# Kernel optimization log

Measured on AMD Instinct MI355X. Metric: run time of the kernel, lower is better.

The kernel has to match this reference:

```python
import jax, jax.numpy as jnp
import numpy as np
from jax import lax

ANGRES = 5


def _conv(x, w, stride=(1, 1), pad=((1, 1), (1, 1)), dil=(1, 1)):
    return lax.conv_general_dilated(x, w, stride, pad, rhs_dilation=dil,
                                    dimension_numbers=('NCHW', 'OIHW', 'NCHW'))


def _lrelu(x):
    return jnp.where(x >= 0, x, 0.1 * x)


def _block_s(x, w):
    # SAI input: split into 5x5 grid of (sh,sw) views, conv each view, emit MacPI-interleaved layout
    B, C, H, W = x.shape
    sh, sw = H // 5, W // 5
    p = x.reshape(B, C, 5, sh, 5, sw).transpose(0, 2, 4, 1, 3, 5).reshape(B * 25, C, sh, sw)
    y = _conv(p, w).reshape(B, 5, 5, C, sh, sw)
    # (B,bi,bj,C,sh,sw) -> (B,C,sh,bi,sw,bj) -> (B,C,H,W)   [torch permute(0,3,4,1,5,2)]
    return y.transpose(0, 3, 4, 1, 5, 2).reshape(B, C, H, W)


def _block_a(x, w):
    # MacPI input: conv each 5x5 macropixel independently (zero pad at block edges)
    B, C, H, W = x.shape
    nh, nw = H // 5, W // 5
    p = x.reshape(B, C, nh, 5, nw, 5).transpose(0, 2, 4, 1, 3, 5).reshape(B * nh * nw, C, 5, 5)
    y = _conv(p, w)
    return y.reshape(B, nh, nw, C, 5, 5).transpose(0, 3, 1, 4, 2, 5).reshape(B, C, H, W)


def _epi(x, w1, w2, a):
    # EPI conv: [1,3a] kernel, stride [1,a], pad [0,a]; then 1x1 to a*C; then 1D pixel shuffle on W
    y = _lrelu(_conv(x, w1, stride=(1, a), pad=((0, 0), (a, a))))
    y = _lrelu(_conv(y, w2, pad=((0, 0), (0, 0))))
    B, aC, H, Wa = y.shape
    C = aC // a
    return y.reshape(B, a, C, H, Wa).transpose(0, 2, 3, 4, 1).reshape(B, C, H, Wa * a)


def _att_fuse(buf, alpha, gamma, beta, eps=1e-5):
    # covariance-based GLU attention over the N=4 branches
    B, NC, H, W = buf.shape
    N = 4
    C = NC // N
    x5 = buf.reshape(B, N, C, H, W)
    xr = x5.reshape(B, N, C * H * W)
    M = xr.shape[-1]
    xc = xr - jnp.mean(xr, axis=-1, keepdims=True)
    cov = jnp.einsum('bnm,bkm->bnk', xc, xc) * (alpha / (M - 1))  # [B,N,N]
    norm = cov / jnp.sqrt(jnp.mean(cov * cov, axis=(1, 2), keepdims=True) + eps)
    g = gamma * norm + beta
    att = g * jax.nn.sigmoid(g)  # GLU of duplicated halves
    out = jnp.einsum('bnk,bkm->bnm', att, xr).reshape(B, N, C, H, W) + x5
    return out.reshape(B, NC, H, W)


def _mac2sai(x, a):
    B, C, HU, WV = x.shape
    h, w = HU // a, WV // a
    return x.reshape(B, C, a, h, a, w).transpose(0, 1, 3, 5, 2, 4).reshape(B, C, h * a, w * a)


def _tsfefb(x, x1, ws, wa, we1, we2, al, ga, be, wf1, wf2, a):
    feaSpa = _lrelu(_block_s(x1, ws))
    feaAng = _lrelu(_block_a(x, wa))
    feaH = _epi(x, we1, we2, a)
    feaV = jnp.transpose(_epi(jnp.transpose(x, (0, 1, 3, 2)), we1, we2, a), (0, 1, 3, 2))
    buf = jnp.concatenate([feaSpa, feaAng, feaH, feaV], axis=1)
    out = _att_fuse(buf, al, ga, be)
    y = _lrelu(_conv(out, wf1, pad=((0, 0), (0, 0))))
    y = _conv(y, wf2, pad=((a, a), (a, a)), dil=(a, a))
    return y + x


def setup_inputs() -> dict:
    key = jax.random.key(0)
    ks = jax.random.split(key, 12)
    B, C, a, n = 4, 64, ANGRES, 4
    H = W = a * 32  # 160

    def w(k, shape):
        fan_in = float(np.prod(shape[2:]))
        return jax.random.normal(k, shape, jnp.float32) / np.float32(np.sqrt(fan_in))

    return {
        'x': jax.random.normal(ks[0], (B, C, H, W), jnp.float32),
        'x1': jax.random.normal(ks[1], (B, C, H, W), jnp.float32),
        'w_spa': w(ks[2], (n, C, C, 3, 3)),
        'w_ang': w(ks[3], (n, C, C, 3, 3)),
        'w_epi1': w(ks[4], (n, C, C, 1, 3 * a)),
        'w_epi2': w(ks[5], (n, a * C, C, 1, 1)),
        'alpha': jnp.ones((n,), jnp.float32),
        'gamma': 0.1 * jax.random.normal(ks[6], (n,), jnp.float32),
        'beta': 0.1 * jax.random.normal(ks[7], (n,), jnp.float32),
        'w_fuse1': w(ks[8], (n, C, 4 * C, 1, 1)),
        'w_fuse2': w(ks[9], (n, C, C, 3, 3)),
    }


def reference(x, x1, w_spa, w_ang, w_epi1, w_epi2, alpha, gamma, beta, w_fuse1, w_fuse2):
    a = ANGRES
    buf, buf1 = x, x1
    for i in range(w_spa.shape[0]):
        buf = _tsfefb(buf, buf1, w_spa[i], w_ang[i], w_epi1[i], w_epi2[i],
                      alpha[i], gamma[i], beta[i], w_fuse1[i], w_fuse2[i], a)
        buf1 = _mac2sai(buf, a)
    return buf
```

## Files before the change

### kernel.cpp

```cpp
#include <hip/hip_runtime.h>

__device__ __forceinline__ float lrelu(float v){ return v >= 0.f ? v : 0.1f*v; }


__global__ __launch_bounds__(256) void k_spa(const float* __restrict__ buf1, const float* __restrict__ w,
                                             float* __restrict__ out){
  const int P = blockIdx.x;
  const int within = P >> 3, cog = within & 7, tsel = within >> 3;
  const int tg = (P & 7)*25 + tsel;
  const int b = tg / 50, r2 = tg % 50;
  const int view = r2 >> 1, half = r2 & 1;
  const int bi = view / 5, bj = view % 5;
  const int th0 = half*16;
  const int tid = threadIdx.x;
  __shared__ float plane[2][18*38];
  for (int idx=tid; idx<2*18*38; idx+=256) ((float*)plane)[idx]=0.f;
  float acc[2][8];
  #pragma unroll
  for (int k=0;k<2;k++)
    #pragma unroll
    for (int c=0;c<8;c++) acc[k][c]=0.f;
  const float* src = buf1 + (size_t)b*1638400 + bi*32*160 + bj*32;
  const float* wb = w + (size_t)(cog*8)*576;
  const int sr = tid >> 3, sq = (tid & 7)*4;
  const int vr = th0 - 1 + sr;
  const bool rowok = (tid < 144) && ((unsigned)vr < 32u);
  __syncthreads();
  if (rowok)
    *(float4*)&plane[0][sr*38 + 4 + sq] = *(const float4*)(src + vr*160 + sq);
  __syncthreads();
  const int lr = tid >> 5, c = tid & 31;
  for (int ci=0; ci<64; ci++){
    float4 nx;
    const bool ld = rowok && (ci < 63);
    if (ld) nx = *(const float4*)(src + (size_t)(ci+1)*25600 + vr*160 + sq);
    const float* P2 = plane[ci & 1];
    float t0[9], t1[9];
    {
      const float* pp = &P2[lr*38 + c + 3];
      t0[0]=pp[0];  t0[1]=pp[1];  t0[2]=pp[2];
      t0[3]=pp[38]; t0[4]=pp[39]; t0[5]=pp[40];
      t0[6]=pp[76]; t0[7]=pp[77]; t0[8]=pp[78];
      const float* qq = pp + 8*38;
      t1[0]=qq[0];  t1[1]=qq[1];  t1[2]=qq[2];
      t1[3]=qq[38]; t1[4]=qq[39]; t1[5]=qq[40];
      t1[6]=qq[76]; t1[7]=qq[77]; t1[8]=qq[78];
    }
    #pragma unroll
    for (int co=0;co<8;co++){
      const float* wp = wb + (size_t)co*576 + ci*9;
      float w0=wp[0],w1=wp[1],w2=wp[2],w3=wp[3],w4=wp[4],w5=wp[5],w6=wp[6],w7=wp[7],w8=wp[8];
      acc[0][co] += t0[0]*w0+t0[1]*w1+t0[2]*w2+t0[3]*w3+t0[4]*w4
                  + t0[5]*w5+t0[6]*w6+t0[7]*w7+t0[8]*w8;
      acc[1][co] += t1[0]*w0+t1[1]*w1+t1[2]*w2+t1[3]*w3+t1[4]*w4
                  + t1[5]*w5+t1[6]*w6+t1[7]*w7+t1[8]*w8;
    }
    if (ld) *(float4*)&plane[(ci+1)&1][sr*38 + 4 + sq] = nx;
    __syncthreads();
  }
  #pragma unroll
  for (int k=0;k<2;k++){
    int si = th0 + lr + k*8;
    int h = si*5 + bi, wq = c*5 + bj;
    #pragma unroll
    for (int co=0;co<8;co++){
      int ch = b*64 + cog*8 + co;
      out[(size_t)ch*25600 + h*160 + wq] = lrelu(acc[k][co]);
    }
  }
}

__global__ __launch_bounds__(320) void k_ang(const float* __restrict__ bufA, const float* __restrict__ w,
                                             float* __restrict__ out){
  const int P = blockIdx.x;
  const int within = P >> 3, cog = within & 15, tsel = within >> 4;
  const int tg = (P & 7)*8 + tsel;
  const int b = tg >> 4, mip = tg & 15;
  const int tid = threadIdx.x;
  __shared__ float lds[2][2296];
  for (int i=tid; i<2*2296; i+=320) ((float*)lds)[i] = 0.f;

  const int u = tid >> 6, mi_l = (tid >> 5) & 1, mp = tid & 31;
  int ro[3];
  #pragma unroll
  for (int du=0; du<3; du++)
    ro[du] = mi_l*1148 + (u+du)*164 + mp*5;
  const bool st1 = tid < 80;
  const int rr0 = tid/40,       q0 = tid%40;
  const int rr1 = (tid+320)/40, q1 = (tid+320)%40;
  const int dst0 = (rr0/5)*1148 + (1 + rr0%5)*164 + q0*4;
  const int dst1 = (rr1/5)*1148 + (1 + rr1%5)*164 + q1*4;
  const float* src = bufA + (size_t)b*1638400 + (size_t)(mip*10)*160;
  const float* wb = w + (size_t)(cog*4)*576;

  float acc[4][5];
  #pragma unroll
  for (int co=0;co<4;co++)
    #pragma unroll
    for (int v=0;v<5;v++) acc[co][v]=0.f;

  __syncthreads();
  {
    *(float4*)&lds[0][dst0] = *(const float4*)(src + rr0*160 + q0*4);
    if (st1)
      *(float4*)&lds[0][dst1] = *(const float4*)(src + rr1*160 + q1*4);
  }
  __syncthreads();
  for (int ci=0; ci<64; ci++){
    float4 n0, n1;
    if (ci < 63){
      n0 = *(const float4*)(src + (size_t)(ci+1)*25600 + rr0*160 + q0*4);
      if (st1) n1 = *(const float4*)(src + (size_t)(ci+1)*25600 + rr1*160 + q1*4);
    }
    const float* Pb = lds[ci & 1];
    float c[3][5];
    #pragma unroll
    for (int du=0;du<3;du++){
      const float* rp = &Pb[ro[du]];
      c[du][0]=rp[0]; c[du][1]=rp[1]; c[du][2]=rp[2]; c[du][3]=rp[3]; c[du][4]=rp[4];
    }
    #pragma unroll
    for (int co=0;co<4;co++){
      const float* wp = wb + (size_t)co*576 + ci*9;
      float w0=wp[0],w1=wp[1],w2=wp[2],w3=wp[3],w4=wp[4],w5=wp[5],w6=wp[6],w7=wp[7],w8=wp[8];
      acc[co][0] += c[0][0]*w1 + c[0][1]*w2
                  + c[1][0]*w4 + c[1][1]*w5
                  + c[2][0]*w7 + c[2][1]*w8;
      acc[co][1] += c[0][0]*w0 + c[0][1]*w1 + c[0][2]*w2
                  + c[1][0]*w3 + c[1][1]*w4 + c[1][2]*w5
                  + c[2][0]*w6 + c[2][1]*w7 + c[2][2]*w8;
      acc[co][2] += c[0][1]*w0 + c[0][2]*w1 + c[0][3]*w2
                  + c[1][1]*w3 + c[1][2]*w4 + c[1][3]*w5
                  + c[2][1]*w6 + c[2][2]*w7 + c[2][3]*w8;
      acc[co][3] += c[0][2]*w0 + c[0][3]*w1 + c[0][4]*w2
                  + c[1][2]*w3 + c[1][3]*w4 + c[1][4]*w5
                  + c[2][2]*w6 + c[2][3]*w7 + c[2][4]*w8;
      acc[co][4] += c[0][3]*w0 + c[0][4]*w1
                  + c[1][3]*w3 + c[1][4]*w4
                  + c[2][3]*w6 + c[2][4]*w7;
    }
    if (ci < 63){
      float* Q = lds[(ci+1)&1];
      *(float4*)&Q[dst0] = n0;
      if (st1) *(float4*)&Q[dst1] = n1;
    }
    __syncthreads();
  }
  const int h = (mip*2 + mi_l)*5 + u;
  const int wc0 = mp*5;
  #pragma unroll
  for (int co=0;co<4;co++){
    int ch = b*64 + cog*4 + co;
    float* op = out + (size_t)ch*25600 + (size_t)h*160 + wc0;
    op[0]=lrelu(acc[co][0]); op[1]=lrelu(acc[co][1]); op[2]=lrelu(acc[co][2]);
    op[3]=lrelu(acc[co][3]); op[4]=lrelu(acc[co][4]);
  }
}

__global__ __launch_bounds__(320) void k_epi(const float* __restrict__ bufA, const float* __restrict__ we1,
                                             const float* __restrict__ we2, float* __restrict__ out){
  const int bb = blockIdx.x >> 1, half = blockIdx.x & 1;
  const int b = bb / 160, hw = bb % 160;
  const int tid = threadIdx.x;
  __shared__ float rowp[64*96];
  __shared__ float y1s[64*16];
  const int lofs = half ? 0 : 8;
  const int xofs = half ? 72 : 0;
  for (int ft=tid; ft<1408; ft+=320){
    int ci = ft/22, q = ft - ci*22;
    *(float4*)&rowp[ci*96 + lofs + q*4] =
      *(const float4*)(bufA + (size_t)b*1638400 + (size_t)ci*25600 + (size_t)hw*160 + xofs + q*4);
  }
  for (int idx=tid; idx<512; idx+=320){
    int ci = idx>>3, j = idx&7;
    rowp[ci*96 + (half ? 88+j : j)] = 0.f;
  }
  __syncthreads();
  if (tid < 256){
    const int co = tid >> 2, wvl0 = (tid & 3)*4;
    const int a0 = 2 + wvl0*5;
    float acc[4];
    #pragma unroll
    for (int j=0;j<4;j++) acc[j]=0.f;
    const float* wp0 = we1 + (size_t)co*960;
    for (int ci=0; ci<64; ci++){
      float fl[32];
      const float* rp = &rowp[ci*96 + a0];
      #pragma unroll
      for (int m=0;m<16;m++) *(float2*)&fl[2*m] = *(const float2*)&rp[2*m];
      const float* wp = wp0 + ci*15;
      #pragma unroll
      for (int t=0;t<15;t++){
        float wt = wp[t];
        #pragma unroll
        for (int j=0;j<4;j++) acc[j] += fl[1 + j*5 + t]*wt;
      }
    }
    #pragma unroll
    for (int j=0;j<4;j++) y1s[co*16 + wvl0 + j] = lrelu(acc[j]);
  }
  __syncthreads();
  {
    const int oc = tid, kk = oc >> 6, c = oc & 63;
    float a2[16];
    #pragma unroll
    for (int wv=0;wv<16;wv++) a2[wv]=0.f;
    const float* wp = we2 + (size_t)oc*64;
    for (int ci=0; ci<64; ci++){
      float wt = wp[ci];
      const float* yp = &y1s[ci*16];
      #pragma unroll
      for (int wv=0; wv<16; wv++) a2[wv] += yp[wv]*wt;
    }
    float* y2s = rowp;
    #pragma unroll
    for (int wv=0; wv<16; wv++) y2s[c*84 + wv*5 + kk] = lrelu(a2[wv]);
  }
  __syncthreads();
  {
    const float* y2s = rowp;
    for (int k=0;k<4;k++){
      int f = (tid + k*320)*4;
      int c = f/80, rr = f - c*80;
      *(float4*)(out + (size_t)(b*64+c)*25600 + (size_t)hw*160 + half*80 + rr)
        = *(const float4*)&y2s[c*84+rr];
    }
  }
}

__global__ __launch_bounds__(256) void k_permV(const float* __restrict__ tmp, float* __restrict__ dst){
  const int bc = blockIdx.x;
  const int ti = blockIdx.y / 5, tj = blockIdx.y % 5;
  const int hw0 = ti*32, r0 = tj*32;
  const int lx = threadIdx.x & 31, ly = threadIdx.x >> 5;
  __shared__ float tile[32][33];
  const float* in = tmp + (size_t)bc*25600;
  float* outp = dst + (size_t)bc*25600;
  for (int yy=ly; yy<32; yy+=8)
    tile[yy][lx] = in[(size_t)(hw0+yy)*160 + r0 + lx];
  __syncthreads();
  for (int yy=ly; yy<32; yy+=8)
    outp[(size_t)(r0+yy)*160 + hw0 + lx] = tile[lx][yy];
}

__global__ __launch_bounds__(256) void k_permM(const float* __restrict__ A, float* __restrict__ dst){
  const int bc = blockIdx.x >> 5, hh = blockIdx.x & 31;
  const int tid = threadIdx.x;
  __shared__ float rows[5*160];
  const float* in = A + (size_t)bc*25600;
  if (tid < 200){
    int ai = tid/40, q = (tid - ai*40)*4;
    *(float4*)&rows[ai*160 + q] = *(const float4*)(in + (size_t)(ai*32+hh)*160 + q);
  }
  __syncthreads();
  float* outp = dst + (size_t)bc*25600 + (size_t)hh*800;
  for (int t=tid; t<800; t+=256){
    int ww = t/25, r2 = t - ww*25, ai = r2/5, aj = r2 - ai*5;
    outp[t] = rows[ai*160 + aj*32 + ww];
  }
}

__global__ __launch_bounds__(256) void k_red(const float* __restrict__ b0, const float* __restrict__ b1,
                                             const float* __restrict__ b2, const float* __restrict__ b3,
                                             float* __restrict__ part){
  const int b = blockIdx.y, blk = blockIdx.x;
  const int tid = threadIdx.x;
  const size_t off = (size_t)b*1638400 + (size_t)blk*25600;
  float s0=0,s1=0,s2=0,s3=0;
  float p00=0,p01=0,p02=0,p03=0,p11=0,p12=0,p13=0,p22=0,p23=0,p33=0;
  for (int it=0; it<25; it++){
    size_t m = off + it*1024 + tid*4;
    float4 x0 = *(const float4*)(b0+m);
    float4 x1 = *(const float4*)(b1+m);
    float4 x2 = *(const float4*)(b2+m);
    float4 x3 = *(const float4*)(b3+m);
    s0 += (x0.x+x0.y)+(x0.z+x0.w);
    s1 += (x1.x+x1.y)+(x1.z+x1.w);
    s2 += (x2.x+x2.y)+(x2.z+x2.w);
    s3 += (x3.x+x3.y)+(x3.z+x3.w);
    p00 += x0.x*x0.x+x0.y*x0.y+x0.z*x0.z+x0.w*x0.w;
    p01 += x0.x*x1.x+x0.y*x1.y+x0.z*x1.z+x0.w*x1.w;
    p02 += x0.x*x2.x+x0.y*x2.y+x0.z*x2.z+x0.w*x2.w;
    p03 += x0.x*x3.x+x0.y*x3.y+x0.z*x3.z+x0.w*x3.w;
    p11 += x1.x*x1.x+x1.y*x1.y+x1.z*x1.z+x1.w*x1.w;
    p12 += x1.x*x2.x+x1.y*x2.y+x1.z*x2.z+x1.w*x2.w;
    p13 += x1.x*x3.x+x1.y*x3.y+x1.z*x3.z+x1.w*x3.w;
    p22 += x2.x*x2.x+x2.y*x2.y+x2.z*x2.z+x2.w*x2.w;
    p23 += x2.x*x3.x+x2.y*x3.y+x2.z*x3.z+x2.w*x3.w;
    p33 += x3.x*x3.x+x3.y*x3.y+x3.z*x3.z+x3.w*x3.w;
  }
  float vals[14] = {s0,s1,s2,s3,p00,p01,p02,p03,p11,p12,p13,p22,p23,p33};
  __shared__ float red[4][14];
  int lane = tid & 63, wv = tid >> 6;
  #pragma unroll
  for (int j=0;j<14;j++){
    float v = vals[j];
    #pragma unroll
    for (int o=32;o>0;o>>=1) v += __shfl_down(v,o,64);
    if (lane==0) red[wv][j]=v;
  }
  __syncthreads();
  if (tid<14) part[((size_t)b*64+blk)*16 + tid] = red[0][tid]+red[1][tid]+red[2][tid]+red[3][tid];
}

__global__ __launch_bounds__(256) void k_attW(const float* __restrict__ part,
        const float* __restrict__ alpha, const float* __restrict__ gamma, const float* __restrict__ beta,
        int iblk, const float* __restrict__ wf1, float* __restrict__ Weff){
  const int b = blockIdx.x, tid = threadIdx.x;
  __shared__ float st[14];
  __shared__ float att[16];
  if (tid<14){
    float t=0;
    for (int blk=0;blk<64;blk++) t += part[((size_t)b*64+blk)*16 + tid];
    st[tid]=t;
  }
  __syncthreads();
  if (tid==0){
    const float M = 1638400.f;
    float s[4] = {st[0],st[1],st[2],st[3]};
    float S[4][4];
    S[0][0]=st[4];  S[0][1]=S[1][0]=st[5];  S[0][2]=S[2][0]=st[6];  S[0][3]=S[3][0]=st[7];
    S[1][1]=st[8];  S[1][2]=S[2][1]=st[9];  S[1][3]=S[3][1]=st[10];
    S[2][2]=st[11]; S[2][3]=S[3][2]=st[12]; S[3][3]=st[13];
    float al=alpha[iblk], ga=gamma[iblk], be=beta[iblk];
    float scale = al/(M-1.f);
    float cov[4][4], ss=0.f;
    for (int n=0;n<4;n++) for (int k=0;k<4;k++){
      float c = (S[n][k] - s[n]*s[k]/M)*scale;
      cov[n][k]=c; ss += c*c;
    }
    float rms = sqrtf(ss/16.f + 1e-5f);
    for (int n=0;n<4;n++) for (int k=0;k<4;k++){
      float g = ga*cov[n][k]/rms + be;
      att[n*4+k] = g/(1.f+expf(-g));
    }
  }
  __syncthreads();
  for (int idx=tid; idx<16384; idx+=256){
    int co=idx>>8, kc=idx&255, k=kc>>6, c=kc&63;
    float v = wf1[co*256+kc];
    #pragma unroll
    for (int n=0;n<4;n++) v += att[n*4+k]*wf1[co*256+n*64+c];
    Weff[(size_t)b*16384+idx] = v;
  }
}

__global__ __launch_bounds__(256) void k_fuse1(const float* b0, const float* __restrict__ b1,
                                               const float* __restrict__ b2, const float* __restrict__ b3,
                                               const float* __restrict__ Weff, float* y64){
  const int tile = blockIdx.x, b = blockIdx.y;
  const int px0 = tile*64;
  const int tid = threadIdx.x;
  const int ti = tid >> 4, tj = tid & 15;
  __shared__ float xs[64][68];
  __shared__ float wt[64][68];
  float acc[4][4];
  #pragma unroll
  for (int i=0;i<4;i++)
    #pragma unroll
    for (int j=0;j<4;j++) acc[i][j]=0.f;
  const float* bptr[4] = {b0,b1,b2,b3};
  for (int kb=0; kb<4; kb++){
    const float* xbk = bptr[kb] + (size_t)b*1638400 + px0;
    const float* wb = Weff + (size_t)b*16384 + kb*64;
    __syncthreads();
    for (int idx=tid; idx<4096; idx+=256){
      int kc=idx>>6, px=idx&63;
      xs[kc][px] = xbk[(size_t)kc*25600 + px];
    }
    for (int idx=tid; idx<4096; idx+=256){
      int co=idx>>6, k2=idx&63;
      wt[k2][co] = wb[co*256 + k2];
    }
    __syncthreads();
    for (int k2=0;k2<64;k2++){
      float4 a = *(const float4*)&wt[k2][ti*4];
      float4 v = *(const float4*)&xs[k2][tj*4];
      acc[0][0]+=a.x*v.x; acc[0][1]+=a.x*v.y; acc[0][2]+=a.x*v.z; acc[0][3]+=a.x*v.w;
      acc[1][0]+=a.y*v.x; acc[1][1]+=a.y*v.y; acc[1][2]+=a.y*v.z; acc[1][3]+=a.y*v.w;
      acc[2][0]+=a.z*v.x; acc[2][1]+=a.z*v.y; acc[2][2]+=a.z*v.z; acc[2][3]+=a.z*v.w;
      acc[3][0]+=a.w*v.x; acc[3][1]+=a.w*v.y; acc[3][2]+=a.w*v.z; acc[3][3]+=a.w*v.w;
    }
  }
  #pragma unroll
  for (int i=0;i<4;i++){
    int co = ti*4 + i;
    float4 o = make_float4(lrelu(acc[i][0]), lrelu(acc[i][1]), lrelu(acc[i][2]), lrelu(acc[i][3]));
    *(float4*)(y64 + ((size_t)(b*64+co))*25600 + px0 + tj*4) = o;
  }
}

template<int FINAL>
__global__ __launch_bounds__(256) void k_fuse2(const float* __restrict__ y64, const float* resid,
                                               const float* __restrict__ w, float* outp){
  const int P = blockIdx.x;
  const int within = P >> 3, cog = within & 7, tsel = within >> 3;
  const int tg = (P & 7)*25 + tsel;
  const int b = tg / 50, tile = tg % 50;
  const int th0 = (tile/5)*16, tw0 = (tile%5)*32;
  const int tid = threadIdx.x;
  __shared__ float plane[2][26*48];
  float acc[2][8];
  #pragma unroll
  for (int k=0;k<2;k++)
    #pragma unroll
    for (int c=0;c<8;c++) acc[k][c]=0.f;
  const float* src = y64 + (size_t)b*1638400;
  const float* wb = w + (size_t)(cog*8)*576;
  const int s0r = tid/12,        s0c = tid - (tid/12)*12;
  const int s1i = tid + 256;
  const int s1r = s1i/12,        s1c = s1i - (s1i/12)*12;
  const bool has1 = tid < 56;
  const int g0h = th0 - 5 + s0r, g0w = tw0 - 8 + s0c*4;
  const int g1h = th0 - 5 + s1r, g1w = tw0 - 8 + s1c*4;
  const bool v0 = ((unsigned)g0h < 160u) && ((unsigned)g0w < 160u);
  const bool v1 = has1 && ((unsigned)g1h < 160u) && ((unsigned)g1w < 160u);
  const int go0 = g0h*160 + g0w, go1 = g1h*160 + g1w;
  const int d0 = s0r*48 + s0c*4, d1 = s1r*48 + s1c*4;
  const float4 z4 = make_float4(0.f,0.f,0.f,0.f);
  {
    float4 x0 = v0 ? *(const float4*)(src + go0) : z4;
    *(float4*)&plane[0][d0] = x0;
    if (has1){
      float4 x1 = v1 ? *(const float4*)(src + go1) : z4;
      *(float4*)&plane[0][d1] = x1;
    }
  }
  __syncthreads();
  const int lr = tid >> 5, c = tid & 31;
  const int tap = lr*48 + c + 3;
  for (int ci=0; ci<64; ci++){
    float4 n0, n1;
    if (ci < 63){
      const float* sN = src + (size_t)(ci+1)*25600;
      n0 = v0 ? *(const float4*)(sN + go0) : z4;
      if (has1) n1 = v1 ? *(const float4*)(sN + go1) : z4;
    }
    const float* Pb = plane[ci & 1];
    float t0[9], t1[9];
    {
      const float* pp = &Pb[tap];
      t0[0]=pp[0];      t0[1]=pp[5];      t0[2]=pp[10];
      t0[3]=pp[240];    t0[4]=pp[245];    t0[5]=pp[250];
      t0[6]=pp[480];    t0[7]=pp[485];    t0[8]=pp[490];
      const float* qq = pp + 8*48;
      t1[0]=qq[0];      t1[1]=qq[5];      t1[2]=qq[10];
      t1[3]=qq[240];    t1[4]=qq[245];    t1[5]=qq[250];
      t1[6]=qq[480];    t1[7]=qq[485];    t1[8]=qq[490];
    }
    #pragma unroll
    for (int co=0;co<8;co++){
      const float* wp = wb + (size_t)co*576 + ci*9;
      float w0=wp[0],w1=wp[1],w2=wp[2],w3=wp[3],w4=wp[4],w5=wp[5],w6=wp[6],w7=wp[7],w8=wp[8];
      acc[0][co] += t0[0]*w0+t0[1]*w1+t0[2]*w2+t0[3]*w3+t0[4]*w4
                  + t0[5]*w5+t0[6]*w6+t0[7]*w7+t0[8]*w8;
      acc[1][co] += t1[0]*w0+t1[1]*w1+t1[2]*w2+t1[3]*w3+t1[4]*w4
                  + t1[5]*w5+t1[6]*w6+t1[7]*w7+t1[8]*w8;
    }
    if (ci < 63){
      float* Q = plane[(ci+1)&1];
      *(float4*)&Q[d0] = n0;
      if (has1) *(float4*)&Q[d1] = n1;
    }
    __syncthreads();
  }
  #pragma unroll
  for (int k=0;k<2;k++){
    int h = th0 + lr + k*8, wq = tw0 + c;
    #pragma unroll
    for (int co=0;co<8;co++){
      int cg = cog*8 + co;
      size_t base = ((size_t)(b*64+cg)*160 + h)*160 + wq;
      outp[base] = acc[k][co] + resid[base];
    }
  }
}

extern "C" void kernel_launch(void* const* d_in, const int* in_sizes, int n_in,
                              void* d_out, int out_size, void* d_ws, size_t ws_size,
                              hipStream_t stream){
  const float* x    = (const float*)d_in[0];
  const float* x1   = (const float*)d_in[1];
  const float* wspa = (const float*)d_in[2];
  const float* wang = (const float*)d_in[3];
  const float* we1  = (const float*)d_in[4];
  const float* we2  = (const float*)d_in[5];
  const float* al   = (const float*)d_in[6];
  const float* ga   = (const float*)d_in[7];
  const float* be   = (const float*)d_in[8];
  const float* wf1  = (const float*)d_in[9];
  const float* wf2  = (const float*)d_in[10];

  char* ws = (char*)d_ws;
  const size_t SLOT = 26214400;
  float* A  = (float*)(ws);
  float* Bv = (float*)(ws +   SLOT);
  float* T1 = (float*)(ws + 2*SLOT);
  float* T2 = (float*)(ws + 3*SLOT);
  float* part = (float*)(ws + 4*SLOT);
  float* Weff = (float*)(ws + 4*SLOT + 16384);
  float* D = (float*)d_out;

  for (int i=0;i<4;i++){
    const float* Asrc  = (i==0) ? x  : (const float*)A;
    const float* B1src = (i==0) ? x1 : (const float*)Bv;
    k_permV<<<dim3(256,25),256,0,stream>>>(Asrc, D);
    k_epi<<<1280,320,0,stream>>>(D, we1 + (size_t)i*61440, we2 + (size_t)i*20480, T2);
    k_spa<<<1600,256,0,stream>>>(B1src, wspa + (size_t)i*36864, T1);
    k_permV<<<dim3(256,25),256,0,stream>>>(T2, Bv);
    k_ang<<<1024,320,0,stream>>>(Asrc, wang + (size_t)i*36864, T2);
    k_epi<<<1280,320,0,stream>>>(Asrc, we1 + (size_t)i*61440, we2 + (size_t)i*20480, D);
    k_red<<<dim3(64,4),256,0,stream>>>(T1, T2, D, Bv, part);
    k_attW<<<4,256,0,stream>>>(part, al, ga, be, i, wf1 + (size_t)i*16384, Weff);
    k_fuse1<<<dim3(400,4),256,0,stream>>>(T1, T2, D, Bv, Weff, T1);
    if (i<3){
      k_fuse2<0><<<1600,256,0,stream>>>(T1, Asrc, wf2 + (size_t)i*36864, A);
      k_permM<<<8192,256,0,stream>>>(A, Bv);
    } else {
      k_fuse2<1><<<1600,256,0,stream>>>(T1, Asrc, wf2 + (size_t)i*36864, D);
    }
  }
}
```

Before: 2.780 ms.

## Repack 3x3 conv weights ci-major and give k_spa adjacent output rows

Adds a pre-pass kernel that transposes the spatial, angular and fuse2 3x3 weights into [ci][co][9] order, so each input-channel iteration reads one contiguous span of weights for the block's output channels instead of strided rows. Separately, k_spa now assigns each thread two vertically adjacent output rows and loads a 4x3 shared-memory window instead of two separate 3x3 windows, sharing the overlapping rows. The cost is one extra launch and extra workspace for the repacked weights each call.

```diff
diff --git a/kernel.cpp b/kernel.cpp
--- a/kernel.cpp
+++ b/kernel.cpp
@@ -2,6 +2,17 @@
 
 __device__ __forceinline__ float lrelu(float v){ return v >= 0.f ? v : 0.1f*v; }
 
+
+__global__ __launch_bounds__(256) void k_wrep(const float* __restrict__ wspa, const float* __restrict__ wang,
+                                              const float* __restrict__ wf2, float* __restrict__ outp){
+  int id = blockIdx.x*256 + threadIdx.x;
+  int t = id / 147456, r = id - t*147456;
+  int i = r / 36864,  e = r - i*36864;
+  int ci = e / 576,   r3 = e - ci*576;
+  int co = r3 / 9,    j = r3 - co*9;
+  const float* src = (t==0 ? wspa : (t==1 ? wang : wf2));
+  outp[id] = src[(size_t)i*36864 + co*576 + ci*9 + j];
+}
 
 __global__ __launch_bounds__(256) void k_spa(const float* __restrict__ buf1, const float* __restrict__ w,
                                              float* __restrict__ out){
@@ -21,7 +32,6 @@
     #pragma unroll
     for (int c=0;c<8;c++) acc[k][c]=0.f;
   const float* src = buf1 + (size_t)b*1638400 + bi*32*160 + bj*32;
-  const float* wb = w + (size_t)(cog*8)*576;
   const int sr = tid >> 3, sq = (tid & 7)*4;
   const int vr = th0 - 1 + sr;
   const bool rowok = (tid < 144) && ((unsigned)vr < 32u);
@@ -29,38 +39,36 @@
   if (rowok)
     *(float4*)&plane[0][sr*38 + 4 + sq] = *(const float4*)(src + vr*160 + sq);
   __syncthreads();
-  const int lr = tid >> 5, c = tid & 31;
+  const int lr2 = tid >> 5, c = tid & 31;
   for (int ci=0; ci<64; ci++){
     float4 nx;
     const bool ld = rowok && (ci < 63);
     if (ld) nx = *(const float4*)(src + (size_t)(ci+1)*25600 + vr*160 + sq);
     const float* P2 = plane[ci & 1];
-    float t0[9], t1[9];
+    float g[4][3];
     {
-      const float* pp = &P2[lr*38 + c + 3];
-      t0[0]=pp[0];  t0[1]=pp[1];  t0[2]=pp[2];
-      t0[3]=pp[38]; t0[4]=pp[39]; t0[5]=pp[40];
-      t0[6]=pp[76]; t0[7]=pp[77]; t0[8]=pp[78];
-      const float* qq = pp + 8*38;
-      t1[0]=qq[0];  t1[1]=qq[1];  t1[2]=qq[2];
-      t1[3]=qq[38]; t1[4]=qq[39]; t1[5]=qq[40];
-      t1[6]=qq[76]; t1[7]=qq[77]; t1[8]=qq[78];
-    }
+      const float* pp = &P2[(2*lr2)*38 + c + 3];
+      g[0][0]=pp[0];   g[0][1]=pp[1];   g[0][2]=pp[2];
+      g[1][0]=pp[38];  g[1][1]=pp[39];  g[1][2]=pp[40];
+      g[2][0]=pp[76];  g[2][1]=pp[77];  g[2][2]=pp[78];
+      g[3][0]=pp[114]; g[3][1]=pp[115]; g[3][2]=pp[116];
+    }
+    const float* wrow = w + ci*576 + cog*72;
     #pragma unroll
     for (int co=0;co<8;co++){
-      const float* wp = wb + (size_t)co*576 + ci*9;
+      const float* wp = wrow + co*9;
       float w0=wp[0],w1=wp[1],w2=wp[2],w3=wp[3],w4=wp[4],w5=wp[5],w6=wp[6],w7=wp[7],w8=wp[8];
-      acc[0][co] += t0[0]*w0+t0[1]*w1+t0[2]*w2+t0[3]*w3+t0[4]*w4
-                  + t0[5]*w5+t0[6]*w6+t0[7]*w7+t0[8]*w8;
-      acc[1][co] += t1[0]*w0+t1[1]*w1+t1[2]*w2+t1[3]*w3+t1[4]*w4
-                  + t1[5]*w5+t1[6]*w6+t1[7]*w7+t1[8]*w8;
+      acc[0][co] += g[0][0]*w0+g[0][1]*w1+g[0][2]*w2+g[1][0]*w3+g[1][1]*w4
+                  + g[1][2]*w5+g[2][0]*w6+g[2][1]*w7+g[2][2]*w8;
+      acc[1][co] += g[1][0]*w0+g[1][1]*w1+g[1][2]*w2+g[2][0]*w3+g[2][1]*w4
+                  + g[2][2]*w5+g[3][0]*w6+g[3][1]*w7+g[3][2]*w8;
     }
     if (ld) *(float4*)&plane[(ci+1)&1][sr*38 + 4 + sq] = nx;
     __syncthreads();
   }
   #pragma unroll
   for (int k=0;k<2;k++){
-    int si = th0 + lr + k*8;
+    int si = th0 + 2*lr2 + k;
     int h = si*5 + bi, wq = c*5 + bj;
     #pragma unroll
     for (int co=0;co<8;co++){
@@ -91,7 +99,6 @@
   const int dst0 = (rr0/5)*1148 + (1 + rr0%5)*164 + q0*4;
   const int dst1 = (rr1/5)*1148 + (1 + rr1%5)*164 + q1*4;
   const float* src = bufA + (size_t)b*1638400 + (size_t)(mip*10)*160;
-  const float* wb = w + (size_t)(cog*4)*576;
 
   float acc[4][5];
   #pragma unroll
@@ -119,9 +126,10 @@
       const float* rp = &Pb[ro[du]];
       c[du][0]=rp[0]; c[du][1]=rp[1]; c[du][2]=rp[2]; c[du][3]=rp[3]; c[du][4]=rp[4];
     }
+    const float* wrow = w + ci*576 + cog*36;
     #pragma unroll
     for (int co=0;co<4;co++){
-      const float* wp = wb + (size_t)co*576 + ci*9;
+      const float* wp = wrow + co*9;
       float w0=wp[0],w1=wp[1],w2=wp[2],w3=wp[3],w4=wp[4],w5=wp[5],w6=wp[6],w7=wp[7],w8=wp[8];
       acc[co][0] += c[0][0]*w1 + c[0][1]*w2
                   + c[1][0]*w4 + c[1][1]*w5
@@ -406,7 +414,6 @@
     #pragma unroll
     for (int c=0;c<8;c++) acc[k][c]=0.f;
   const float* src = y64 + (size_t)b*1638400;
-  const float* wb = w + (size_t)(cog*8)*576;
   const int s0r = tid/12,        s0c = tid - (tid/12)*12;
   const int s1i = tid + 256;
   const int s1r = s1i/12,        s1c = s1i - (s1i/12)*12;
@@ -448,9 +455,10 @@
       t1[3]=qq[240];    t1[4]=qq[245];    t1[5]=qq[250];
       t1[6]=qq[480];    t1[7]=qq[485];    t1[8]=qq[490];
     }
+    const float* wrow = w + ci*576 + cog*72;
     #pragma unroll
     for (int co=0;co<8;co++){
-      const float* wp = wb + (size_t)co*576 + ci*9;
+      const float* wp = wrow + co*9;
       float w0=wp[0],w1=wp[1],w2=wp[2],w3=wp[3],w4=wp[4],w5=wp[5],w6=wp[6],w7=wp[7],w8=wp[8];
       acc[0][co] += t0[0]*w0+t0[1]*w1+t0[2]*w2+t0[3]*w3+t0[4]*w4
                   + t0[5]*w5+t0[6]*w6+t0[7]*w7+t0[8]*w8;
@@ -499,25 +507,31 @@
   float* T2 = (float*)(ws + 3*SLOT);
   float* part = (float*)(ws + 4*SLOT);
   float* Weff = (float*)(ws + 4*SLOT + 16384);
+  float* Wrep = (float*)(ws + 4*SLOT + 16384 + 262144);
+  float* WspaR = Wrep;
+  float* WangR = Wrep + 147456;
+  float* Wf2R  = Wrep + 2*147456;
   float* D = (float*)d_out;
+
+  k_wrep<<<1728,256,0,stream>>>(wspa, wang, wf2, Wrep);
 
   for (int i=0;i<4;i++){
     const float* Asrc  = (i==0) ? x  : (const float*)A;
     const float* B1src = (i==0) ? x1 : (const float*)Bv;
     k_permV<<<dim3(256,25),256,0,stream>>>(Asrc, D);
     k_epi<<<1280,320,0,stream>>>(D, we1 + (size_t)i*61440, we2 + (size_t)i*20480, T2);
-    k_spa<<<1600,256,0,stream>>>(B1src, wspa + (size_t)i*36864, T1);
+    k_spa<<<1600,256,0,stream>>>(B1src, WspaR + (size_t)i*36864, T1);
     k_permV<<<dim3(256,25),256,0,stream>>>(T2, Bv);
-    k_ang<<<1024,320,0,stream>>>(Asrc, wang + (size_t)i*36864, T2);
+    k_ang<<<1024,320,0,stream>>>(Asrc, WangR + (size_t)i*36864, T2);
     k_epi<<<1280,320,0,stream>>>(Asrc, we1 + (size_t)i*61440, we2 + (size_t)i*20480, D);
     k_red<<<dim3(64,4),256,0,stream>>>(T1, T2, D, Bv, part);
     k_attW<<<4,256,0,stream>>>(part, al, ga, be, i, wf1 + (size_t)i*16384, Weff);
     k_fuse1<<<dim3(400,4),256,0,stream>>>(T1, T2, D, Bv, Weff, T1);
     if (i<3){
-      k_fuse2<0><<<1600,256,0,stream>>>(T1, Asrc, wf2 + (size_t)i*36864, A);
+      k_fuse2<0><<<1600,256,0,stream>>>(T1, Asrc, Wf2R + (size_t)i*36864, A);
       k_permM<<<8192,256,0,stream>>>(A, Bv);
     } else {
-      k_fuse2<1><<<1600,256,0,stream>>>(T1, Asrc, wf2 + (size_t)i*36864, D);
-    }
-  }
-}
+      k_fuse2<1><<<1600,256,0,stream>>>(T1, Asrc, Wf2R + (size_t)i*36864, D);
+    }
+  }
+}
```

Result: no change. 2.807 ms (+1.0%).
